# Performance work log

Measured on AMD Instinct MI355X. Metric: run time of the kernel, lower is better.

The kernel has to match this reference:

```python
import jax, jax.numpy as jnp
import numpy as np

N = 100000   # nodes
E = 300000   # directed edges
D = 256      # emb_dim
G = 4000     # graphs
L = 5        # num_layer
F_IN = 40    # num_atom_features
NUM_BOND_TYPE = 6       # pretrain-gnns convention; self-loop bond type = 4
NUM_BOND_DIRECTION = 3
EPS = 1e-5


def setup_inputs() -> dict:
    key = jax.random.key(0)
    ks = jax.random.split(key, 32)
    s = 0.05
    inp = {}
    inp["x"] = jax.random.normal(ks[0], (N, F_IN), jnp.float32)
    inp["edge_index"] = jax.random.randint(ks[1], (2, E), 0, N)
    inp["edge_attr"] = jax.random.randint(ks[2], (E, 2), 0, 3)
    inp["batch"] = jnp.sort(jax.random.randint(ks[3], (N,), 0, G))
    # atom embedding (Linear + ReLU)
    inp["embW"] = jax.random.normal(ks[4], (F_IN, D), jnp.float32) * s
    inp["embB"] = jnp.zeros((D,), jnp.float32)
    # per-layer GINConv params (stacked over layers)
    inp["ee1"] = jax.random.normal(ks[5], (L, NUM_BOND_TYPE, D), jnp.float32) * s
    inp["ee2"] = jax.random.normal(ks[6], (L, NUM_BOND_DIRECTION, D), jnp.float32) * s
    inp["W1"] = jax.random.normal(ks[7], (L, D, 2 * D), jnp.float32) * s
    inp["b1"] = jnp.zeros((L, 2 * D), jnp.float32)
    inp["W2"] = jax.random.normal(ks[8], (L, 2 * D, D), jnp.float32) * s
    inp["b2"] = jnp.zeros((L, D), jnp.float32)
    inp["bn_g"] = jnp.ones((L, D), jnp.float32)
    inp["bn_b"] = jnp.zeros((L, D), jnp.float32)
    # MLP head: 256 -> 256 -> 128 -> 64 -> 32 -> 1
    dims = [D, D, D // 2, D // 4, D // 8]
    kk = jax.random.split(ks[9], 5)
    for i in range(4):
        inp[f"hW{i}"] = jax.random.normal(kk[i], (dims[i], dims[i + 1]), jnp.float32) * s
        inp[f"hb{i}"] = jnp.zeros((dims[i + 1],), jnp.float32)
    inp["hWo"] = jax.random.normal(kk[4], (dims[4], 1), jnp.float32) * s
    inp["hbo"] = jnp.zeros((1,), jnp.float32)
    return inp


def reference(x, edge_index, edge_attr, batch, embW, embB, ee1, ee2, W1, b1, W2, b2,
              bn_g, bn_b, hW0, hb0, hW1, hb1, hW2, hb2, hW3, hb3, hWo, hbo):
    src, dst = edge_index[0], edge_index[1]
    ea0, ea1 = edge_attr[:, 0], edge_attr[:, 1]
    # x_embedding1: Linear + ReLU
    h = jax.nn.relu(x @ embW + embB)
    for l in range(L):
        # GINConv: gather source features + edge embeddings, scatter-add to dst
        msg = h[src] + ee1[l][ea0] + ee2[l][ea1]        # [E, D]
        agg = jax.ops.segment_sum(msg, dst, num_segments=N)
        # self-loop message (bond type 4, direction 0)
        agg = agg + h + ee1[l][4] + ee2[l][0]
        # GIN MLP: Linear(D, 2D) -> ReLU -> Linear(2D, D)
        h2 = jax.nn.relu(agg @ W1[l] + b1[l]) @ W2[l] + b2[l]
        # BatchNorm1d (training-mode batch statistics, biased variance)
        mu = h2.mean(axis=0)
        var = h2.var(axis=0)
        h2 = (h2 - mu) * jax.lax.rsqrt(var + EPS) * bn_g[l] + bn_b[l]
        if l < L - 1:
            h2 = jax.nn.relu(h2)
        # dropout with drop_ratio=0.0 -> identity
        h = h2
    # JK == 'last'
    node_rep = h
    # global_mean_pool
    counts = jnp.maximum(jax.ops.segment_sum(jnp.ones((N,), node_rep.dtype), batch, num_segments=G), 1.0)
    mol = jax.ops.segment_sum(node_rep, batch, num_segments=G) / counts[:, None]
    # MLP head
    z = jax.nn.relu(mol @ hW0 + hb0)
    z = jax.nn.relu(z @ hW1 + hb1)
    z = jax.nn.relu(z @ hW2 + hb2)
    z = jax.nn.relu(z @ hW3 + hb3)
    out = z @ hWo + hbo
    return out.reshape(-1)  # MolEmbed.view(-1), num_tasks == 1
```

## Files before the change

### kernel.cpp

```cpp
#include <hip/hip_runtime.h>
#include <hip/hip_bf16.h>

#define NN 100000
#define EE 300000
#define GG 4000
#define LL 5
#define GPB 4
#define SC_CHUNK 1024
#define SC_NB ((NN + SC_CHUNK - 1) / SC_CHUNK)

typedef _Float16 half8  __attribute__((ext_vector_type(8)));
typedef _Float16 half4v __attribute__((ext_vector_type(4)));
typedef float    f32x4  __attribute__((ext_vector_type(4)));

__device__ inline short f2h(float f) {
    _Float16 h = (_Float16)f;
    short s; __builtin_memcpy(&s, &h, 2); return s;
}

__device__ inline void async_load16(const void* g, void* l) {
    __builtin_amdgcn_global_load_lds(
        (const __attribute__((address_space(1))) unsigned int*)g,
        (__attribute__((address_space(3))) unsigned int*)l, 16, 0, 0);
}

__global__ __launch_bounds__(256) void k_count(
    int* __restrict__ deg, const int* __restrict__ ei)
{
    int e = blockIdx.x * 256 + threadIdx.x;
    if (e < EE) atomicAdd(&deg[ei[EE + e]], 1);
}

__global__ __launch_bounds__(256) void k_scan_partial(
    int* __restrict__ partial, const int* __restrict__ deg)
{
    int b = blockIdx.x, t = threadIdx.x;
    int lane = t & 63, w = t >> 6;
    int base = b * SC_CHUNK + t * 4;
    int s = 0;
#pragma unroll
    for (int j = 0; j < 4; ++j) {
        int i = base + j;
        if (i < NN) s += deg[i];
    }
#pragma unroll
    for (int off = 1; off < 64; off <<= 1) s += __shfl_xor(s, off, 64);
    __shared__ int ws[4];
    if (lane == 0) ws[w] = s;
    __syncthreads();
    if (t == 0) partial[b] = ws[0] + ws[1] + ws[2] + ws[3];
}

__global__ __launch_bounds__(128) void k_scan_base(
    int* __restrict__ bases, int* __restrict__ offs, const int* __restrict__ partial)
{
    int t = threadIdx.x;
    int lane = t & 63, w = t >> 6;
    int p = (t < SC_NB) ? partial[t] : 0;
    int x = p;
#pragma unroll
    for (int off = 1; off < 64; off <<= 1) {
        int nb = __shfl_up(x, off, 64);
        if (lane >= off) x += nb;
    }
    __shared__ int w0tot;
    if (t == 63) w0tot = x;
    __syncthreads();
    if (w == 1) x += w0tot;
    if (t < SC_NB) bases[t] = x - p;
    if (t == 0) offs[NN] = EE;
}

__global__ __launch_bounds__(256) void k_scan_final(
    int* __restrict__ offs, int* __restrict__ cursor,
    const int* __restrict__ deg, const int* __restrict__ bases)
{
    int b = blockIdx.x, t = threadIdx.x;
    int lane = t & 63, w = t >> 6;
    int base = b * SC_CHUNK + t * 4;
    int v[4], pre[4], run = 0;
#pragma unroll
    for (int j = 0; j < 4; ++j) {
        int i = base + j;
        v[j] = (i < NN) ? deg[i] : 0;
        pre[j] = run;
        run += v[j];
    }
    int x = run;
#pragma unroll
    for (int off = 1; off < 64; off <<= 1) {
        int nb = __shfl_up(x, off, 64);
        if (lane >= off) x += nb;
    }
    int tex = x - run;
    __shared__ int ws[4];
    if (lane == 63) ws[w] = x;
    __syncthreads();
    int woff = 0;
    for (int k = 0; k < 4; ++k) if (k < w) woff += ws[k];
    int tbase = bases[b] + woff + tex;
#pragma unroll
    for (int j = 0; j < 4; ++j) {
        int i = base + j;
        if (i < NN) { offs[i] = tbase + pre[j]; cursor[i] = tbase + pre[j]; }
    }
}

__global__ __launch_bounds__(256) void k_fill(
    int* __restrict__ csr, int* __restrict__ cursor,
    const int* __restrict__ ei, const int* __restrict__ ea)
{
    int e = blockIdx.x * 256 + threadIdx.x;
    if (e >= EE) return;
    int s = ei[e];
    int d = ei[EE + e];
    int c = ea[2 * e] * 3 + ea[2 * e + 1];
    int slot = atomicAdd(&cursor[d], 1);
    csr[slot] = s | (c << 20);
}

__global__ __launch_bounds__(256) void k_goffs(
    int* __restrict__ goffs, const int* __restrict__ batch)
{
    int n = blockIdx.x * 256 + threadIdx.x;
    if (n >= NN) return;
    int b = batch[n];
    int bp = (n == 0) ? -1 : batch[n - 1];
    for (int g = bp + 1; g <= b; ++g) goffs[g] = n;
    if (n == NN - 1)
        for (int g = b + 1; g <= GG; ++g) goffs[g] = NN;
}

__global__ __launch_bounds__(256) void k_combo(
    float* __restrict__ tbl, const float* __restrict__ ee1, const float* __restrict__ ee2)
{
    int c = blockIdx.x;
    int l = blockIdx.y;
    int t = threadIdx.x;
    int i1 = (c < 9) ? c / 3 : 4;
    int i2 = (c < 9) ? c % 3 : 0;
    tbl[((size_t)l * 10 + c) * 256 + t] =
        ee1[((size_t)l * 6 + i1) * 256 + t] + ee2[((size_t)l * 3 + i2) * 256 + t];
}

__global__ __launch_bounds__(256) void k_pack_emb(
    _Float16* __restrict__ Wep, const float* __restrict__ embW)
{
    int idx = blockIdx.x * 256 + threadIdx.x;
    int ks = idx >> 13, r = idx & 8191;
    int n = r >> 5, kk = r & 31;
    int k = ks * 32 + kk;
    float v = (k < 40) ? embW[(size_t)k * 256 + n] : 0.f;
    Wep[idx] = (_Float16)v;
}

__global__ __launch_bounds__(256) void k_embed_mfma(
    _Float16* __restrict__ H, const float* __restrict__ x,
    const _Float16* __restrict__ Wep, const float* __restrict__ bias)
{
    __shared__ __align__(16) char smem[67584];
    _Float16* As = (_Float16*)smem;
    _Float16* Bs = (_Float16*)(smem + 16384);
    _Float16* Cs = (_Float16*)smem;

    const int t = threadIdx.x;
    const int w = t >> 6, lane = t & 63;
    const int quad = lane >> 4, l16 = lane & 15;
    const int wr = w >> 1, wc = w & 1;
    const int gm0 = blockIdx.x * 128;

#pragma unroll
    for (int i = 0; i < 8; ++i) {
        int u = i * 256 + t;
        async_load16((const char*)Wep + u * 16, (char*)Bs + u * 16);
    }

    {
        int row = t >> 1, half = t & 1;
        int rg = gm0 + row; if (rg > NN - 1) rg = NN - 1;
        const float* xp = x + (size_t)rg * 40 + half * 20;
        float v[20];
#pragma unroll
        for (int j = 0; j < 5; ++j) {
            float4 q = *(const float4*)(xp + j * 4);
            v[j * 4 + 0] = q.x; v[j * 4 + 1] = q.y; v[j * 4 + 2] = q.z; v[j * 4 + 3] = q.w;
        }
#pragma unroll
        for (int j = 0; j < 20; ++j) {
            int col = half * 20 + j;
            int ks = col >> 5, kk = col & 31;
            As[ks * 4096 + row * 32 + kk] = (_Float16)v[j];
        }
        int kb = 8 + half * 12;
#pragma unroll
        for (int j = 0; j < 12; ++j)
            As[4096 + row * 32 + kb + j] = (_Float16)0.f;
    }

    float biasreg[8];
#pragma unroll
    for (int nt = 0; nt < 8; ++nt)
        biasreg[nt] = bias[wc * 128 + nt * 16 + l16];

    f32x4 acc[4][8];
#pragma unroll
    for (int i = 0; i < 4; ++i)
#pragma unroll
        for (int j = 0; j < 8; ++j) acc[i][j] = (f32x4){0.f, 0.f, 0.f, 0.f};

    __syncthreads();

#pragma unroll
    for (int ks = 0; ks < 2; ++ks) {
        half8 af[4], bfr[8];
#pragma unroll
        for (int mt = 0; mt < 4; ++mt)
            af[mt] = *(const half8*)(As + ks * 4096 + (wr * 64 + mt * 16 + l16) * 32 + quad * 8);
#pragma unroll
        for (int nt = 0; nt < 8; ++nt)
            bfr[nt] = *(const half8*)(Bs + ks * 8192 + (wc * 128 + nt * 16 + l16) * 32 + quad * 8);
#pragma unroll
        for (int mt = 0; mt < 4; ++mt)
#pragma unroll
            for (int nt = 0; nt < 8; ++nt)
                acc[mt][nt] = __builtin_amdgcn_mfma_f32_16x16x32_f16(
                    af[mt], bfr[nt], acc[mt][nt], 0, 0, 0);
    }

    __syncthreads();
#pragma unroll
    for (int mt = 0; mt < 4; ++mt)
#pragma unroll
        for (int nt = 0; nt < 8; ++nt)
#pragma unroll
            for (int r = 0; r < 4; ++r) {
                int row = wr * 64 + mt * 16 + quad * 4 + r;
                int col = wc * 128 + nt * 16 + l16;
                Cs[row * 264 + col] = (_Float16)fmaxf(acc[mt][nt][r] + biasreg[nt], 0.f);
            }
    __syncthreads();
#pragma unroll
    for (int i = 0; i < 16; ++i) {
        int u = i * 256 + t;
        int m = u >> 5, ch = u & 31;
        int grow = gm0 + m;
        if (grow < NN)
            *(int4*)(H + (size_t)grow * 256 + ch * 8) =
                *(const int4*)(Cs + m * 264 + ch * 8);
    }
}

template <int AFF>
__global__ __launch_bounds__(256) void k_aggregate(
    _Float16* __restrict__ agg, const _Float16* __restrict__ hin,
    const int* __restrict__ offs, const int* __restrict__ csr,
    const float* __restrict__ tbl,
    const float* __restrict__ scale, const float* __restrict__ shift)
{
    int t = threadIdx.x;
    int w = t >> 6, lane = t & 63;
    int n = blockIdx.x * 4 + w;

    f32x4 sc, sh;
    if (AFF) { sc = ((const f32x4*)scale)[lane]; sh = ((const f32x4*)shift)[lane]; }
    const f32x4* tb4 = (const f32x4*)tbl;

    half4v hv = *(const half4v*)(hin + (size_t)n * 256 + lane * 4);
    f32x4 acc = tb4[9 * 64 + lane];
#pragma unroll
    for (int i = 0; i < 4; ++i) {
        float v = (float)hv[i];
        if (AFF) v = fmaf(v, sc[i], sh[i]);
        acc[i] += fmaxf(v, 0.f);
    }

    int o0 = offs[n], o1 = offs[n + 1];
    for (int j = o0; j < o1; ++j) {
        int entry = csr[j];
        int s = entry & 0xFFFFF;
        int c = entry >> 20;
        half4v gv = *(const half4v*)(hin + (size_t)s * 256 + lane * 4);
        f32x4 tv = tb4[c * 64 + lane];
#pragma unroll
        for (int i = 0; i < 4; ++i) {
            float v = (float)gv[i];
            if (AFF) v = fmaf(v, sc[i], sh[i]);
            acc[i] += fmaxf(v, 0.f) + tv[i];
        }
    }

    half4v o;
#pragma unroll
    for (int i = 0; i < 4; ++i) o[i] = (_Float16)acc[i];
    *(half4v*)(agg + (size_t)n * 256 + lane * 4) = o;
}

__global__ __launch_bounds__(256) void k_pack(
    short* __restrict__ dst, const float* __restrict__ src, int K, int Nsz)
{
    int nb = blockIdx.x, kb = blockIdx.y, l = blockIdx.z;
    int t = threadIdx.x;
    __shared__ float T[32][65];
    const float* s = src + ((size_t)l * K + kb * 32) * Nsz + nb * 64;
#pragma unroll
    for (int i = 0; i < 8; ++i) {
        int idx = i * 256 + t;
        int kk = idx >> 6, nl = idx & 63;
        T[kk][nl] = s[(size_t)kk * Nsz + nl];
    }
    __syncthreads();
    int nl = t >> 2, kq = t & 3;
    union { short s[8]; int4 v; } o;
#pragma unroll
    for (int j = 0; j < 8; ++j) o.s[j] = f2h(T[kq * 8 + j][nl]);
    short* d = dst + (((size_t)l * (K / 32) + kb) * Nsz + nb * 64 + nl) * 32 + kq * 8;
    *(int4*)d = o.v;
}

__global__ __launch_bounds__(256, 3) void k_fused_mlp(
    _Float16* __restrict__ H2, const _Float16* __restrict__ A,
    const short* __restrict__ W1p, const float* __restrict__ b1,
    const short* __restrict__ W2p, const float* __restrict__ b2,
    float* __restrict__ stats)
{
    __shared__ __align__(16) char smem[40960];
    _Float16* As = (_Float16*)smem;
    _Float16* Us = (_Float16*)(smem + 32768);
    _Float16* Cs = (_Float16*)smem;

    const int t = threadIdx.x;
    const int w = t >> 6, lane = t & 63;
    const int quad = lane >> 4, l16 = lane & 15;
    const int bm = blockIdx.x;
    const int gm0 = bm * 64;
    const int swz = l16 & 7;

#pragma unroll
    for (int i = 0; i < 8; ++i) {
        int u = i * 256 + t;
        int row = u >> 5;
        int gcol = (u & 31) ^ (row & 7);
        int grow = gm0 + row; if (grow > NN - 1) grow = NN - 1;
        async_load16(A + (size_t)grow * 256 + gcol * 8, (char*)As + u * 16);
    }

    const _Float16* w1w = (const _Float16*)W1p + ((size_t)(w * 16 + l16)) * 32 + quad * 8;
    const _Float16* w2w = (const _Float16*)W2p + ((size_t)(w * 64 + l16)) * 32 + quad * 8;

    half8 w1buf[8];
#pragma unroll
    for (int i = 0; i < 8; ++i)
        w1buf[i] = *(const half8*)(w1w + ((size_t)i * 512) * 32);
    half8 w2k0[4];
#pragma unroll
    for (int nt = 0; nt < 4; ++nt)
        w2k0[nt] = *(const half8*)(w2w + ((size_t)nt * 16) * 32);

    f32x4 acc2[4][4];
#pragma unroll
    for (int i = 0; i < 4; ++i)
#pragma unroll
        for (int j = 0; j < 4; ++j) acc2[i][j] = (f32x4){0.f, 0.f, 0.f, 0.f};

    __syncthreads();

    for (int j = 0; j < 8; ++j) {
        f32x4 acc1[4];
#pragma unroll
        for (int b = 0; b < 4; ++b) acc1[b] = (f32x4){0.f, 0.f, 0.f, 0.f};

#pragma unroll
        for (int kb = 0; kb < 8; ++kb) {
            int slotA = (kb * 4 + quad) ^ swz;
            half8 b1f[4];
#pragma unroll
            for (int urt = 0; urt < 4; ++urt)
                b1f[urt] = *(const half8*)(As + (urt * 16 + l16) * 256 + slotA * 8);
#pragma unroll
            for (int urt = 0; urt < 4; ++urt)
                acc1[urt] = __builtin_amdgcn_mfma_f32_16x16x32_f16(
                    w1buf[kb], b1f[urt], acc1[urt], 0, 0, 0);
        }

        {
            int ucl = w * 16 + quad * 4;
            float4 bv = *(const float4*)(b1 + j * 64 + ucl);
            int G = ucl >> 3;
            int hs = quad & 1;
#pragma unroll
            for (int urt = 0; urt < 4; ++urt) {
                int ur = urt * 16 + l16;
                int S = G ^ (ur & 7);
                half4v o;
                o[0] = (_Float16)fmaxf(acc1[urt][0] + bv.x, 0.f);
                o[1] = (_Float16)fmaxf(acc1[urt][1] + bv.y, 0.f);
                o[2] = (_Float16)fmaxf(acc1[urt][2] + bv.z, 0.f);
                o[3] = (_Float16)fmaxf(acc1[urt][3] + bv.w, 0.f);
                *(half4v*)(Us + ur * 64 + S * 8 + hs * 4) = o;
            }
        }
        asm volatile("s_waitcnt lgkmcnt(0)" ::: "memory");
        __builtin_amdgcn_s_barrier();
        __builtin_amdgcn_sched_barrier(0);

        half8 a2n[4];
#pragma unroll
        for (int nt = 0; nt < 4; ++nt)
            a2n[nt] = *(const half8*)(w2w + ((size_t)(j * 2 + 1) * 256 + nt * 16) * 32);
        if (j < 7) {
#pragma unroll
            for (int i = 0; i < 8; ++i)
                w1buf[i] = *(const half8*)(w1w + ((size_t)i * 512 + (j + 1) * 64) * 32);
        }

        {
            int slotU = quad ^ swz;
            half8 b2f[4];
#pragma unroll
            for (int mt = 0; mt < 4; ++mt)
                b2f[mt] = *(const half8*)(Us + (mt * 16 + l16) * 64 + slotU * 8);
#pragma unroll
            for (int nt = 0; nt < 4; ++nt)
#pragma unroll
                for (int mt = 0; mt < 4; ++mt)
                    acc2[nt][mt] = __builtin_amdgcn_mfma_f32_16x16x32_f16(
                        w2k0[nt], b2f[mt], acc2[nt][mt], 0, 0, 0);
        }
        if (j < 7) {
#pragma unroll
            for (int nt = 0; nt < 4; ++nt)
                w2k0[nt] = *(const half8*)(w2w + ((size_t)(j + 1) * 2 * 256 + nt * 16) * 32);
        }
        {
            int slotU = (4 + quad) ^ swz;
            half8 b2f[4];
#pragma unroll
            for (int mt = 0; mt < 4; ++mt)
                b2f[mt] = *(const half8*)(Us + (mt * 16 + l16) * 64 + slotU * 8);
#pragma unroll
            for (int nt = 0; nt < 4; ++nt)
#pragma unroll
                for (int mt = 0; mt < 4; ++mt)
                    acc2[nt][mt] = __builtin_amdgcn_mfma_f32_16x16x32_f16(
                        a2n[nt], b2f[mt], acc2[nt][mt], 0, 0, 0);
        }
        asm volatile("s_waitcnt lgkmcnt(0)" ::: "memory");
        __builtin_amdgcn_s_barrier();
        __builtin_amdgcn_sched_barrier(0);
    }

    int slot2 = bm & 63;
#pragma unroll
    for (int nt = 0; nt < 4; ++nt) {
        int nb = w * 64 + nt * 16 + quad * 4;
        float4 bv = *(const float4*)(b2 + nb);
        float s1[4] = {0.f, 0.f, 0.f, 0.f};
        float s2[4] = {0.f, 0.f, 0.f, 0.f};
#pragma unroll
        for (int mt = 0; mt < 4; ++mt) {
            int mr = mt * 16 + l16;
            int m = gm0 + mr;
            float v0 = acc2[nt][mt][0] + bv.x;
            float v1 = acc2[nt][mt][1] + bv.y;
            float v2 = acc2[nt][mt][2] + bv.z;
            float v3 = acc2[nt][mt][3] + bv.w;
            half4v o;
            o[0] = (_Float16)v0; o[1] = (_Float16)v1;
            o[2] = (_Float16)v2; o[3] = (_Float16)v3;
            *(half4v*)(Cs + mr * 264 + nb) = o;
            if (m < NN) {
                s1[0] += v0; s1[1] += v1; s1[2] += v2; s1[3] += v3;
                s2[0] += v0 * v0; s2[1] += v1 * v1;
                s2[2] += v2 * v2; s2[3] += v3 * v3;
            }
        }
#pragma unroll
        for (int r = 0; r < 4; ++r) {
            s1[r] += __shfl_xor(s1[r], 1, 64); s2[r] += __shfl_xor(s2[r], 1, 64);
            s1[r] += __shfl_xor(s1[r], 2, 64); s2[r] += __shfl_xor(s2[r], 2, 64);
            s1[r] += __shfl_xor(s1[r], 4, 64); s2[r] += __shfl_xor(s2[r], 4, 64);
            s1[r] += __shfl_xor(s1[r], 8, 64); s2[r] += __shfl_xor(s2[r], 8, 64);
            if (l16 == 0) {
                atomicAdd(&stats[slot2 * 512 + nb + r], s1[r]);
                atomicAdd(&stats[slot2 * 512 + 256 + nb + r], s2[r]);
            }
        }
    }
    __syncthreads();
#pragma unroll
    for (int i = 0; i < 8; ++i) {
        int u = i * 256 + t;
        int m = u >> 5, ch = u & 31;
        int grow = gm0 + m;
        if (grow < NN)
            *(int4*)(H2 + (size_t)grow * 256 + ch * 8) =
                *(const int4*)(Cs + m * 264 + ch * 8);
    }
}

__global__ __launch_bounds__(256) void k_bn_finalize(
    float* __restrict__ scale, float* __restrict__ shift,
    float* __restrict__ stats,
    const float* __restrict__ bn_g, const float* __restrict__ bn_b)
{
    int t = threadIdx.x;
    float s1 = 0.f, s2 = 0.f;
    for (int j = 0; j < 64; ++j) {
        s1 += stats[j * 512 + t];
        s2 += stats[j * 512 + 256 + t];
        stats[j * 512 + t] = 0.f;
        stats[j * 512 + 256 + t] = 0.f;
    }
    float mu  = s1 / (float)NN;
    float var = s2 / (float)NN - mu * mu;
    float sc  = bn_g[t] * rsqrtf(var + 1e-5f);
    scale[t] = sc;
    shift[t] = bn_b[t] - mu * sc;
}

__global__ __launch_bounds__(256) void k_pool(
    float* __restrict__ mol, const _Float16* __restrict__ h,
    const int* __restrict__ goffs,
    const float* __restrict__ scale, const float* __restrict__ shift)
{
    int g = blockIdx.x;
    int t = threadIdx.x;
    int s = goffs[g], e = goffs[g + 1];
    float sum = 0.f;
    for (int n = s; n < e; ++n) sum += (float)h[(size_t)n * 256 + t];
    int c = e - s; if (c < 1) c = 1;
    mol[(size_t)g * 256 + t] = fmaf(sum / (float)c, scale[t], shift[t]);
}

__global__ __launch_bounds__(256) void k_head(
    float* __restrict__ out, const float* __restrict__ mol,
    const float* __restrict__ hW0, const float* __restrict__ hb0,
    const float* __restrict__ hW1, const float* __restrict__ hb1,
    const float* __restrict__ hW2, const float* __restrict__ hb2,
    const float* __restrict__ hW3, const float* __restrict__ hb3,
    const float* __restrict__ hWo, const float* __restrict__ hbo)
{
    __shared__ float za[GPB][256];
    __shared__ float zb[GPB][256];
    const int t = threadIdx.x;
    const int g0 = blockIdx.x * GPB;

#pragma unroll
    for (int g = 0; g < GPB; ++g)
        za[g][t] = mol[(size_t)(g0 + g) * 256 + t];
    __syncthreads();

    {
        float acc[GPB];
#pragma unroll
        for (int g = 0; g < GPB; ++g) acc[g] = 0.f;
        for (int k = 0; k < 256; ++k) {
            float w = hW0[k * 256 + t];
#pragma unroll
            for (int g = 0; g < GPB; ++g) acc[g] = fmaf(za[g][k], w, acc[g]);
        }
        float b = hb0[t];
#pragma unroll
        for (int g = 0; g < GPB; ++g) zb[g][t] = fmaxf(acc[g] + b, 0.f);
    }
    __syncthreads();

    if (t < 128) {
        float acc[GPB];
#pragma unroll
        for (int g = 0; g < GPB; ++g) acc[g] = 0.f;
        for (int k = 0; k < 256; ++k) {
            float w = hW1[k * 128 + t];
#pragma unroll
            for (int g = 0; g < GPB; ++g) acc[g] = fmaf(zb[g][k], w, acc[g]);
        }
        float b = hb1[t];
#pragma unroll
        for (int g = 0; g < GPB; ++g) za[g][t] = fmaxf(acc[g] + b, 0.f);
    }
    __syncthreads();

    if (t < 64) {
        float acc[GPB];
#pragma unroll
        for (int g = 0; g < GPB; ++g) acc[g] = 0.f;
        for (int k = 0; k < 128; ++k) {
            float w = hW2[k * 64 + t];
#pragma unroll
            for (int g = 0; g < GPB; ++g) acc[g] = fmaf(za[g][k], w, acc[g]);
        }
        float b = hb2[t];
#pragma unroll
        for (int g = 0; g < GPB; ++g) zb[g][t] = fmaxf(acc[g] + b, 0.f);
    }
    __syncthreads();

    if (t < 32) {
        float acc[GPB];
#pragma unroll
        for (int g = 0; g < GPB; ++g) acc[g] = 0.f;
        for (int k = 0; k < 64; ++k) {
            float w = hW3[k * 32 + t];
#pragma unroll
            for (int g = 0; g < GPB; ++g) acc[g] = fmaf(zb[g][k], w, acc[g]);
        }
        float b = hb3[t];
#pragma unroll
        for (int g = 0; g < GPB; ++g) za[g][t] = fmaxf(acc[g] + b, 0.f);
    }
    __syncthreads();

    if (t < GPB) {
        float s = hbo[0];
        for (int k = 0; k < 32; ++k) s = fmaf(za[t][k], hWo[k], s);
        out[g0 + t] = s;
    }
}

extern "C" void kernel_launch(void* const* d_in, const int* in_sizes, int n_in,
                              void* d_out, int out_size, void* d_ws, size_t ws_size,
                              hipStream_t stream)
{
    const float* x    = (const float*)d_in[0];
    const int*   ei   = (const int*)d_in[1];
    const int*   ea   = (const int*)d_in[2];
    const int*   batch= (const int*)d_in[3];
    const float* embW = (const float*)d_in[4];
    const float* embB = (const float*)d_in[5];
    const float* ee1  = (const float*)d_in[6];
    const float* ee2  = (const float*)d_in[7];
    const float* W1   = (const float*)d_in[8];
    const float* b1   = (const float*)d_in[9];
    const float* W2   = (const float*)d_in[10];
    const float* b2   = (const float*)d_in[11];
    const float* bng  = (const float*)d_in[12];
    const float* bnb  = (const float*)d_in[13];
    const float* hW0  = (const float*)d_in[14];
    const float* hb0  = (const float*)d_in[15];
    const float* hW1  = (const float*)d_in[16];
    const float* hb1  = (const float*)d_in[17];
    const float* hW2  = (const float*)d_in[18];
    const float* hb2  = (const float*)d_in[19];
    const float* hW3  = (const float*)d_in[20];
    const float* hb3  = (const float*)d_in[21];
    const float* hWo  = (const float*)d_in[22];
    const float* hbo  = (const float*)d_in[23];
    float* out = (float*)d_out;

    char* ws = (char*)d_ws;
    size_t off = 0;
    _Float16* h2buf = (_Float16*)(ws + off); off += (size_t)NN * 256 * 2;
    _Float16* aggbuf= (_Float16*)(ws + off); off += (size_t)NN * 256 * 2;
    short* W1p      = (short*)(ws + off);    off += (size_t)5 * 131072 * 2;
    short* W2p      = (short*)(ws + off);    off += (size_t)5 * 131072 * 2;
    _Float16* Wep   = (_Float16*)(ws + off); off += (size_t)2 * 8192 * 2;
    float* tbl      = (float*)(ws + off);    off += (size_t)5 * 10 * 256 * 4;
    float* stats    = (float*)(ws + off);    off += (size_t)64 * 512 * 4;
    float* scale    = (float*)(ws + off);    off += 256 * 4;
    float* shift    = (float*)(ws + off);    off += 256 * 4;
    float* mol      = (float*)(ws + off);    off += (size_t)GG * 256 * 4;
    int* deg        = (int*)(ws + off);      off += (size_t)NN * 4;
    int* offs       = (int*)(ws + off);      off += (size_t)(NN + 1) * 4;
    int* cursor     = (int*)(ws + off);      off += (size_t)NN * 4;
    int* csr        = (int*)(ws + off);      off += (size_t)EE * 4;
    int* goffs      = (int*)(ws + off);      off += (size_t)(GG + 1) * 4;
    int* partial    = (int*)(ws + off);      off += 128 * 4;
    int* bases      = (int*)(ws + off);      off += 128 * 4;

    hipMemsetAsync(deg, 0, (size_t)NN * 4, stream);
    hipMemsetAsync(stats, 0, (size_t)64 * 512 * 4, stream);
    k_count<<<(EE + 255) / 256, 256, 0, stream>>>(deg, ei);
    k_scan_partial<<<SC_NB, 256, 0, stream>>>(partial, deg);
    k_scan_base<<<1, 128, 0, stream>>>(bases, offs, partial);
    k_scan_final<<<SC_NB, 256, 0, stream>>>(offs, cursor, deg, bases);
    k_fill<<<(EE + 255) / 256, 256, 0, stream>>>(csr, cursor, ei, ea);
    k_goffs<<<(NN + 255) / 256, 256, 0, stream>>>(goffs, batch);
    k_combo<<<dim3(10, 5), 256, 0, stream>>>(tbl, ee1, ee2);
    k_pack<<<dim3(8, 8, 5), 256, 0, stream>>>(W1p, W1, 256, 512);
    k_pack<<<dim3(4, 16, 5), 256, 0, stream>>>(W2p, W2, 512, 256);
    k_pack_emb<<<64, 256, 0, stream>>>(Wep, embW);

    k_embed_mfma<<<782, 256, 0, stream>>>(h2buf, x, Wep, embB);

    const int FB = (NN + 63) / 64;
    for (int l = 0; l < LL; ++l) {
        if (l == 0)
            k_aggregate<0><<<NN / 4, 256, 0, stream>>>(aggbuf, h2buf, offs, csr,
                                                       tbl, scale, shift);
        else
            k_aggregate<1><<<NN / 4, 256, 0, stream>>>(aggbuf, h2buf, offs, csr,
                                                       tbl + (size_t)l * 10 * 256, scale, shift);
        k_fused_mlp<<<FB, 256, 0, stream>>>(h2buf, aggbuf,
                                            W1p + (size_t)l * 131072, b1 + l * 512,
                                            W2p + (size_t)l * 131072, b2 + l * 256, stats);
        k_bn_finalize<<<1, 256, 0, stream>>>(scale, shift, stats, bng + l * 256, bnb + l * 256);
    }

    k_pool<<<GG, 256, 0, stream>>>(mol, h2buf, goffs, scale, shift);
    k_head<<<GG / GPB, 256, 0, stream>>>(out, mol,
                                         hW0, hb0, hW1, hb1, hW2, hb2, hW3, hb3, hWo, hbo);
}
```

Baseline: 973.8 us.

## Fuse neighbor aggregation into per-layer MLP kernel with gather/compute overlap

Removes the separate aggregate kernel and gathers neighbor rows directly into shared memory inside the MLP kernel. Each block now handles two 64-row tiles and gathers the second tile's rows while computing the first tile's GEMMs, which avoids writing the aggregate buffer to global memory and reading it back. The MLP output is written straight to global memory instead of being staged through shared memory, and the two H buffers are ping-ponged across layers. The cost is 72KB of shared memory with occupancy capped at 2 blocks, half as many blocks, and gather latency sitting inside the MFMA loop, which can serialize work.

```diff
diff --git a/kernel.cpp b/kernel.cpp
--- a/kernel.cpp
+++ b/kernel.cpp
@@ -250,51 +250,6 @@
     }
 }
 
-template <int AFF>
-__global__ __launch_bounds__(256) void k_aggregate(
-    _Float16* __restrict__ agg, const _Float16* __restrict__ hin,
-    const int* __restrict__ offs, const int* __restrict__ csr,
-    const float* __restrict__ tbl,
-    const float* __restrict__ scale, const float* __restrict__ shift)
-{
-    int t = threadIdx.x;
-    int w = t >> 6, lane = t & 63;
-    int n = blockIdx.x * 4 + w;
-
-    f32x4 sc, sh;
-    if (AFF) { sc = ((const f32x4*)scale)[lane]; sh = ((const f32x4*)shift)[lane]; }
-    const f32x4* tb4 = (const f32x4*)tbl;
-
-    half4v hv = *(const half4v*)(hin + (size_t)n * 256 + lane * 4);
-    f32x4 acc = tb4[9 * 64 + lane];
-#pragma unroll
-    for (int i = 0; i < 4; ++i) {
-        float v = (float)hv[i];
-        if (AFF) v = fmaf(v, sc[i], sh[i]);
-        acc[i] += fmaxf(v, 0.f);
-    }
-
-    int o0 = offs[n], o1 = offs[n + 1];
-    for (int j = o0; j < o1; ++j) {
-        int entry = csr[j];
-        int s = entry & 0xFFFFF;
-        int c = entry >> 20;
-        half4v gv = *(const half4v*)(hin + (size_t)s * 256 + lane * 4);
-        f32x4 tv = tb4[c * 64 + lane];
-#pragma unroll
-        for (int i = 0; i < 4; ++i) {
-            float v = (float)gv[i];
-            if (AFF) v = fmaf(v, sc[i], sh[i]);
-            acc[i] += fmaxf(v, 0.f) + tv[i];
-        }
-    }
-
-    half4v o;
-#pragma unroll
-    for (int i = 0; i < 4; ++i) o[i] = (_Float16)acc[i];
-    *(half4v*)(agg + (size_t)n * 256 + lane * 4) = o;
-}
-
 __global__ __launch_bounds__(256) void k_pack(
     short* __restrict__ dst, const float* __restrict__ src, int K, int Nsz)
 {
@@ -317,32 +272,67 @@
     *(int4*)d = o.v;
 }
 
-__global__ __launch_bounds__(256, 3) void k_fused_mlp(
-    _Float16* __restrict__ H2, const _Float16* __restrict__ A,
+template <int AFF>
+__device__ __forceinline__ void gather_row(
+    const _Float16* __restrict__ Hsrc, const int* __restrict__ offs,
+    const int* __restrict__ csr, const f32x4* __restrict__ tb4,
+    f32x4 sc, f32x4 sh, int lane, int n, int r, _Float16* dst)
+{
+    if (n > NN - 1) n = NN - 1;
+    f32x4 acc = tb4[9 * 64 + lane];
+    half4v hv = *(const half4v*)(Hsrc + (size_t)n * 256 + lane * 4);
+#pragma unroll
+    for (int q = 0; q < 4; ++q) {
+        float v = (float)hv[q];
+        if (AFF) v = fmaf(v, sc[q], sh[q]);
+        acc[q] += fmaxf(v, 0.f);
+    }
+    int o0 = offs[n], o1 = offs[n + 1];
+    for (int e = o0; e < o1; ++e) {
+        int entry = csr[e];
+        int s = entry & 0xFFFFF;
+        int c = entry >> 20;
+        half4v gv = *(const half4v*)(Hsrc + (size_t)s * 256 + lane * 4);
+        f32x4 tv = tb4[c * 64 + lane];
+#pragma unroll
+        for (int q = 0; q < 4; ++q) {
+            float v = (float)gv[q];
+            if (AFF) v = fmaf(v, sc[q], sh[q]);
+            acc[q] += fmaxf(v, 0.f) + tv[q];
+        }
+    }
+    half4v o;
+#pragma unroll
+    for (int q = 0; q < 4; ++q) o[q] = (_Float16)acc[q];
+    int slot = (lane >> 1) ^ (r & 7);
+    *(half4v*)(dst + r * 256 + slot * 8 + (lane & 1) * 4) = o;
+}
+
+template <int AFF>
+__global__ __launch_bounds__(256, 2) void k_layer(
+    _Float16* __restrict__ Hdst, const _Float16* __restrict__ Hsrc,
+    const int* __restrict__ offs, const int* __restrict__ csr,
+    const float* __restrict__ tbl,
+    const float* __restrict__ scale, const float* __restrict__ shift,
     const short* __restrict__ W1p, const float* __restrict__ b1,
     const short* __restrict__ W2p, const float* __restrict__ b2,
     float* __restrict__ stats)
 {
-    __shared__ __align__(16) char smem[40960];
-    _Float16* As = (_Float16*)smem;
-    _Float16* Us = (_Float16*)(smem + 32768);
-    _Float16* Cs = (_Float16*)smem;
+    __shared__ __align__(16) char smem[73728];
+    _Float16* As0 = (_Float16*)smem;
+    _Float16* As1 = (_Float16*)(smem + 32768);
+    _Float16* Us  = (_Float16*)(smem + 65536);
 
     const int t = threadIdx.x;
     const int w = t >> 6, lane = t & 63;
     const int quad = lane >> 4, l16 = lane & 15;
     const int bm = blockIdx.x;
-    const int gm0 = bm * 64;
     const int swz = l16 & 7;
-
-#pragma unroll
-    for (int i = 0; i < 8; ++i) {
-        int u = i * 256 + t;
-        int row = u >> 5;
-        int gcol = (u & 31) ^ (row & 7);
-        int grow = gm0 + row; if (grow > NN - 1) grow = NN - 1;
-        async_load16(A + (size_t)grow * 256 + gcol * 8, (char*)As + u * 16);
-    }
+    const int ntiles = (bm * 2 + 1 < (NN + 63) / 64) ? 2 : 1;
+
+    f32x4 sc = (f32x4){0.f,0.f,0.f,0.f}, sh = sc;
+    if (AFF) { sc = ((const f32x4*)scale)[lane]; sh = ((const f32x4*)shift)[lane]; }
+    const f32x4* tb4 = (const f32x4*)tbl;
 
     const _Float16* w1w = (const _Float16*)W1p + ((size_t)(w * 16 + l16)) * 32 + quad * 8;
     const _Float16* w2w = (const _Float16*)W2p + ((size_t)(w * 64 + l16)) * 32 + quad * 8;
@@ -356,145 +346,164 @@
     for (int nt = 0; nt < 4; ++nt)
         w2k0[nt] = *(const half8*)(w2w + ((size_t)nt * 16) * 32);
 
-    f32x4 acc2[4][4];
-#pragma unroll
-    for (int i = 0; i < 4; ++i)
-#pragma unroll
-        for (int j = 0; j < 4; ++j) acc2[i][j] = (f32x4){0.f, 0.f, 0.f, 0.f};
-
-    __syncthreads();
-
-    for (int j = 0; j < 8; ++j) {
-        f32x4 acc1[4];
-#pragma unroll
-        for (int b = 0; b < 4; ++b) acc1[b] = (f32x4){0.f, 0.f, 0.f, 0.f};
-
-#pragma unroll
-        for (int kb = 0; kb < 8; ++kb) {
-            int slotA = (kb * 4 + quad) ^ swz;
-            half8 b1f[4];
-#pragma unroll
-            for (int urt = 0; urt < 4; ++urt)
-                b1f[urt] = *(const half8*)(As + (urt * 16 + l16) * 256 + slotA * 8);
-#pragma unroll
-            for (int urt = 0; urt < 4; ++urt)
-                acc1[urt] = __builtin_amdgcn_mfma_f32_16x16x32_f16(
-                    w1buf[kb], b1f[urt], acc1[urt], 0, 0, 0);
-        }
-
-        {
-            int ucl = w * 16 + quad * 4;
-            float4 bv = *(const float4*)(b1 + j * 64 + ucl);
-            int G = ucl >> 3;
-            int hs = quad & 1;
-#pragma unroll
-            for (int urt = 0; urt < 4; ++urt) {
-                int ur = urt * 16 + l16;
-                int S = G ^ (ur & 7);
-                half4v o;
-                o[0] = (_Float16)fmaxf(acc1[urt][0] + bv.x, 0.f);
-                o[1] = (_Float16)fmaxf(acc1[urt][1] + bv.y, 0.f);
-                o[2] = (_Float16)fmaxf(acc1[urt][2] + bv.z, 0.f);
-                o[3] = (_Float16)fmaxf(acc1[urt][3] + bv.w, 0.f);
-                *(half4v*)(Us + ur * 64 + S * 8 + hs * 4) = o;
-            }
-        }
-        asm volatile("s_waitcnt lgkmcnt(0)" ::: "memory");
-        __builtin_amdgcn_s_barrier();
-        __builtin_amdgcn_sched_barrier(0);
-
-        half8 a2n[4];
-#pragma unroll
-        for (int nt = 0; nt < 4; ++nt)
-            a2n[nt] = *(const half8*)(w2w + ((size_t)(j * 2 + 1) * 256 + nt * 16) * 32);
-        if (j < 7) {
-#pragma unroll
-            for (int i = 0; i < 8; ++i)
-                w1buf[i] = *(const half8*)(w1w + ((size_t)i * 512 + (j + 1) * 64) * 32);
-        }
-
-        {
-            int slotU = quad ^ swz;
-            half8 b2f[4];
-#pragma unroll
-            for (int mt = 0; mt < 4; ++mt)
-                b2f[mt] = *(const half8*)(Us + (mt * 16 + l16) * 64 + slotU * 8);
+    {
+        int base = bm * 128;
+#pragma unroll 4
+        for (int i = 0; i < 16; ++i) {
+            int r = w * 16 + i;
+            gather_row<AFF>(Hsrc, offs, csr, tb4, sc, sh, lane, base + r, r, As0);
+        }
+    }
+    asm volatile("s_waitcnt lgkmcnt(0)" ::: "memory");
+    __builtin_amdgcn_s_barrier();
+    __builtin_amdgcn_sched_barrier(0);
+
+#pragma unroll
+    for (int tile = 0; tile < 2; ++tile) {
+        if (tile >= ntiles) break;
+        _Float16* cur = tile ? As1 : As0;
+        _Float16* nxt = tile ? As0 : As1;
+        const int tb0 = bm * 128 + tile * 64;
+        const bool doGather = (tile == 0) && (ntiles == 2);
+
+        f32x4 acc2[4][4];
+#pragma unroll
+        for (int i = 0; i < 4; ++i)
+#pragma unroll
+            for (int jj = 0; jj < 4; ++jj) acc2[i][jj] = (f32x4){0.f, 0.f, 0.f, 0.f};
+
+        for (int j = 0; j < 8; ++j) {
+            f32x4 acc1[4];
+#pragma unroll
+            for (int b = 0; b < 4; ++b) acc1[b] = (f32x4){0.f, 0.f, 0.f, 0.f};
+
+#pragma unroll
+            for (int kb = 0; kb < 8; ++kb) {
+                int slotA = (kb * 4 + quad) ^ swz;
+                half8 b1f[4];
+#pragma unroll
+                for (int urt = 0; urt < 4; ++urt)
+                    b1f[urt] = *(const half8*)(cur + (urt * 16 + l16) * 256 + slotA * 8);
+#pragma unroll
+                for (int urt = 0; urt < 4; ++urt)
+                    acc1[urt] = __builtin_amdgcn_mfma_f32_16x16x32_f16(
+                        w1buf[kb], b1f[urt], acc1[urt], 0, 0, 0);
+            }
+
+            {
+                int ucl = w * 16 + quad * 4;
+                float4 bv = *(const float4*)(b1 + j * 64 + ucl);
+                int G = ucl >> 3;
+                int hs = quad & 1;
+#pragma unroll
+                for (int urt = 0; urt < 4; ++urt) {
+                    int ur = urt * 16 + l16;
+                    int S = G ^ (ur & 7);
+                    half4v o;
+                    o[0] = (_Float16)fmaxf(acc1[urt][0] + bv.x, 0.f);
+                    o[1] = (_Float16)fmaxf(acc1[urt][1] + bv.y, 0.f);
+                    o[2] = (_Float16)fmaxf(acc1[urt][2] + bv.z, 0.f);
+                    o[3] = (_Float16)fmaxf(acc1[urt][3] + bv.w, 0.f);
+                    *(half4v*)(Us + ur * 64 + S * 8 + hs * 4) = o;
+                }
+            }
+            asm volatile("s_waitcnt lgkmcnt(0)" ::: "memory");
+            __builtin_amdgcn_s_barrier();
+            __builtin_amdgcn_sched_barrier(0);
+
+            int jn = (j < 7) ? j + 1 : 0;
+            bool pf = (j < 7) || (tile + 1 < ntiles);
+            half8 a2n[4];
 #pragma unroll
             for (int nt = 0; nt < 4; ++nt)
+                a2n[nt] = *(const half8*)(w2w + ((size_t)(j * 2 + 1) * 256 + nt * 16) * 32);
+            if (pf) {
+#pragma unroll
+                for (int i = 0; i < 8; ++i)
+                    w1buf[i] = *(const half8*)(w1w + ((size_t)i * 512 + jn * 64) * 32);
+            }
+
+            {
+                int slotU = quad ^ swz;
+                half8 b2f[4];
 #pragma unroll
                 for (int mt = 0; mt < 4; ++mt)
-                    acc2[nt][mt] = __builtin_amdgcn_mfma_f32_16x16x32_f16(
-                        w2k0[nt], b2f[mt], acc2[nt][mt], 0, 0, 0);
-        }
-        if (j < 7) {
-#pragma unroll
-            for (int nt = 0; nt < 4; ++nt)
-                w2k0[nt] = *(const half8*)(w2w + ((size_t)(j + 1) * 2 * 256 + nt * 16) * 32);
-        }
-        {
-            int slotU = (4 + quad) ^ swz;
-            half8 b2f[4];
-#pragma unroll
-            for (int mt = 0; mt < 4; ++mt)
-                b2f[mt] = *(const half8*)(Us + (mt * 16 + l16) * 64 + slotU * 8);
-#pragma unroll
-            for (int nt = 0; nt < 4; ++nt)
+                    b2f[mt] = *(const half8*)(Us + (mt * 16 + l16) * 64 + slotU * 8);
+#pragma unroll
+                for (int nt = 0; nt < 4; ++nt)
+#pragma unroll
+                    for (int mt = 0; mt < 4; ++mt)
+                        acc2[nt][mt] = __builtin_amdgcn_mfma_f32_16x16x32_f16(
+                            w2k0[nt], b2f[mt], acc2[nt][mt], 0, 0, 0);
+            }
+            if (pf) {
+#pragma unroll
+                for (int nt = 0; nt < 4; ++nt)
+                    w2k0[nt] = *(const half8*)(w2w + ((size_t)jn * 2 * 256 + nt * 16) * 32);
+            }
+            {
+                int slotU = (4 + quad) ^ swz;
+                half8 b2f[4];
 #pragma unroll
                 for (int mt = 0; mt < 4; ++mt)
-                    acc2[nt][mt] = __builtin_amdgcn_mfma_f32_16x16x32_f16(
-                        a2n[nt], b2f[mt], acc2[nt][mt], 0, 0, 0);
-        }
-        asm volatile("s_waitcnt lgkmcnt(0)" ::: "memory");
-        __builtin_amdgcn_s_barrier();
-        __builtin_amdgcn_sched_barrier(0);
-    }
-
-    int slot2 = bm & 63;
-#pragma unroll
-    for (int nt = 0; nt < 4; ++nt) {
-        int nb = w * 64 + nt * 16 + quad * 4;
-        float4 bv = *(const float4*)(b2 + nb);
-        float s1[4] = {0.f, 0.f, 0.f, 0.f};
-        float s2[4] = {0.f, 0.f, 0.f, 0.f};
-#pragma unroll
-        for (int mt = 0; mt < 4; ++mt) {
-            int mr = mt * 16 + l16;
-            int m = gm0 + mr;
-            float v0 = acc2[nt][mt][0] + bv.x;
-            float v1 = acc2[nt][mt][1] + bv.y;
-            float v2 = acc2[nt][mt][2] + bv.z;
-            float v3 = acc2[nt][mt][3] + bv.w;
-            half4v o;
-            o[0] = (_Float16)v0; o[1] = (_Float16)v1;
-            o[2] = (_Float16)v2; o[3] = (_Float16)v3;
-            *(half4v*)(Cs + mr * 264 + nb) = o;
-            if (m < NN) {
-                s1[0] += v0; s1[1] += v1; s1[2] += v2; s1[3] += v3;
-                s2[0] += v0 * v0; s2[1] += v1 * v1;
-                s2[2] += v2 * v2; s2[3] += v3 * v3;
-            }
-        }
-#pragma unroll
-        for (int r = 0; r < 4; ++r) {
-            s1[r] += __shfl_xor(s1[r], 1, 64); s2[r] += __shfl_xor(s2[r], 1, 64);
-            s1[r] += __shfl_xor(s1[r], 2, 64); s2[r] += __shfl_xor(s2[r], 2, 64);
-            s1[r] += __shfl_xor(s1[r], 4, 64); s2[r] += __shfl_xor(s2[r], 4, 64);
-            s1[r] += __shfl_xor(s1[r], 8, 64); s2[r] += __shfl_xor(s2[r], 8, 64);
-            if (l16 == 0) {
-                atomicAdd(&stats[slot2 * 512 + nb + r], s1[r]);
-                atomicAdd(&stats[slot2 * 512 + 256 + nb + r], s2[r]);
-            }
-        }
-    }
-    __syncthreads();
-#pragma unroll
-    for (int i = 0; i < 8; ++i) {
-        int u = i * 256 + t;
-        int m = u >> 5, ch = u & 31;
-        int grow = gm0 + m;
-        if (grow < NN)
-            *(int4*)(H2 + (size_t)grow * 256 + ch * 8) =
-                *(const int4*)(Cs + m * 264 + ch * 8);
+                    b2f[mt] = *(const half8*)(Us + (mt * 16 + l16) * 64 + slotU * 8);
+#pragma unroll
+                for (int nt = 0; nt < 4; ++nt)
+#pragma unroll
+                    for (int mt = 0; mt < 4; ++mt)
+                        acc2[nt][mt] = __builtin_amdgcn_mfma_f32_16x16x32_f16(
+                            a2n[nt], b2f[mt], acc2[nt][mt], 0, 0, 0);
+            }
+
+            if (doGather) {
+                int r = w * 16 + j * 2;
+                gather_row<AFF>(Hsrc, offs, csr, tb4, sc, sh, lane,
+                                tb0 + 64 + r, r, nxt);
+                gather_row<AFF>(Hsrc, offs, csr, tb4, sc, sh, lane,
+                                tb0 + 64 + r + 1, r + 1, nxt);
+            }
+
+            asm volatile("s_waitcnt lgkmcnt(0)" ::: "memory");
+            __builtin_amdgcn_s_barrier();
+            __builtin_amdgcn_sched_barrier(0);
+        }
+
+        int slot2 = (bm * 2 + tile) & 63;
+#pragma unroll
+        for (int nt = 0; nt < 4; ++nt) {
+            int nb = w * 64 + nt * 16 + quad * 4;
+            float4 bv = *(const float4*)(b2 + nb);
+            float s1[4] = {0.f, 0.f, 0.f, 0.f};
+            float s2[4] = {0.f, 0.f, 0.f, 0.f};
+#pragma unroll
+            for (int mt = 0; mt < 4; ++mt) {
+                int m = tb0 + mt * 16 + l16;
+                float v0 = acc2[nt][mt][0] + bv.x;
+                float v1 = acc2[nt][mt][1] + bv.y;
+                float v2 = acc2[nt][mt][2] + bv.z;
+                float v3 = acc2[nt][mt][3] + bv.w;
+                if (m < NN) {
+                    half4v o;
+                    o[0] = (_Float16)v0; o[1] = (_Float16)v1;
+                    o[2] = (_Float16)v2; o[3] = (_Float16)v3;
+                    *(half4v*)(Hdst + (size_t)m * 256 + nb) = o;
+                    s1[0] += v0; s1[1] += v1; s1[2] += v2; s1[3] += v3;
+                    s2[0] += v0 * v0; s2[1] += v1 * v1;
+                    s2[2] += v2 * v2; s2[3] += v3 * v3;
+                }
+            }
+#pragma unroll
+            for (int r = 0; r < 4; ++r) {
+                s1[r] += __shfl_xor(s1[r], 1, 64); s2[r] += __shfl_xor(s2[r], 1, 64);
+                s1[r] += __shfl_xor(s1[r], 2, 64); s2[r] += __shfl_xor(s2[r], 2, 64);
+                s1[r] += __shfl_xor(s1[r], 4, 64); s2[r] += __shfl_xor(s2[r], 4, 64);
+                s1[r] += __shfl_xor(s1[r], 8, 64); s2[r] += __shfl_xor(s2[r], 8, 64);
+                if (l16 == 0) {
+                    atomicAdd(&stats[slot2 * 512 + nb + r], s1[r]);
+                    atomicAdd(&stats[slot2 * 512 + 256 + nb + r], s2[r]);
+                }
+            }
+        }
     }
 }
 
@@ -682,21 +691,24 @@
 
     k_embed_mfma<<<782, 256, 0, stream>>>(h2buf, x, Wep, embB);
 
-    const int FB = (NN + 63) / 64;
+    _Float16* hb[2] = { h2buf, aggbuf };
+    const int LB = ((NN + 63) / 64 + 1) / 2;
     for (int l = 0; l < LL; ++l) {
+        _Float16* src = hb[l & 1];
+        _Float16* dst = hb[(l + 1) & 1];
         if (l == 0)
-            k_aggregate<0><<<NN / 4, 256, 0, stream>>>(aggbuf, h2buf, offs, csr,
-                                                       tbl, scale, shift);
+            k_layer<0><<<LB, 256, 0, stream>>>(dst, src, offs, csr,
+                tbl, scale, shift,
+                W1p, b1, W2p, b2, stats);
         else
-            k_aggregate<1><<<NN / 4, 256, 0, stream>>>(aggbuf, h2buf, offs, csr,
-                                                       tbl + (size_t)l * 10 * 256, scale, shift);
-        k_fused_mlp<<<FB, 256, 0, stream>>>(h2buf, aggbuf,
-                                            W1p + (size_t)l * 131072, b1 + l * 512,
-                                            W2p + (size_t)l * 131072, b2 + l * 256, stats);
+            k_layer<1><<<LB, 256, 0, stream>>>(dst, src, offs, csr,
+                tbl + (size_t)l * 10 * 256, scale, shift,
+                W1p + (size_t)l * 131072, b1 + l * 512,
+                W2p + (size_t)l * 131072, b2 + l * 256, stats);
         k_bn_finalize<<<1, 256, 0, stream>>>(scale, shift, stats, bng + l * 256, bnb + l * 256);
     }
 
-    k_pool<<<GG, 256, 0, stream>>>(mol, h2buf, goffs, scale, shift);
+    k_pool<<<GG, 256, 0, stream>>>(mol, hb[LL & 1], goffs, scale, shift);
     k_head<<<GG / GPB, 256, 0, stream>>>(out, mol,
                                          hW0, hb0, hW1, hb1, hW2, hb2, hW3, hb3, hWo, hbo);
 }
```

Result: slower. 1.539 ms (+58.0%).
